# Performance work log

Measured on AMD Instinct MI355X. Metric: run time of the kernel, lower is better.

The kernel has to match this reference:

```python
import jax, jax.numpy as jnp
import numpy as np

EPS = 1e-12  # F.normalize eps


def _norm_adj(flow):
    # flow: (T, C, C). PyG gcn_norm with self-loops on the dense cosine-sim graph.
    T = flow.shape[0]
    x = flow.reshape(T, -1)                                  # (T, N)
    xn = x / jnp.clip(jnp.linalg.norm(x, axis=1, keepdims=True), EPS)
    A = xn.T @ xn                                            # (N, N) cosine sims
    N = A.shape[0]
    deg = A.sum(axis=0) + 1.0                                # +1 from added self-loop weight
    dinv = jnp.where(deg > 0, jax.lax.rsqrt(deg), 0.0)
    return (A + jnp.eye(N, dtype=A.dtype)) * dinv[:, None] * dinv[None, :]


def setup_inputs() -> dict:
    key = jax.random.key(0)
    ks = jax.random.split(key, 8)
    B, T, C, E = 8, 24, 64, 32
    H = 32
    O = 32
    return {
        "Flow": jax.random.normal(ks[0], (B, T, C, C), dtype=jnp.float32),
        "Edge": jax.random.normal(ks[1], (B, C, C, E), dtype=jnp.float32),
        "W0": jax.random.normal(ks[2], (E, H), dtype=jnp.float32) * 0.1,
        "b0": jax.random.normal(ks[3], (H,), dtype=jnp.float32) * 0.1,
        "W1": jax.random.normal(ks[4], (H, H), dtype=jnp.float32) * 0.1,
        "b1": jax.random.normal(ks[5], (H,), dtype=jnp.float32) * 0.1,
        "W2": jax.random.normal(ks[6], (H, O), dtype=jnp.float32) * 0.1,
        "b2": jax.random.normal(ks[7], (O,), dtype=jnp.float32) * 0.1,
    }


def reference(Flow, Edge, W0, b0, W1, b1, W2, b2):
    B, C, _, E = Edge.shape

    def per_batch(flow, edge):
        A = _norm_adj(flow)                                  # (N, N)
        x = edge.reshape(C * C, E)                           # (N, E)
        for W, b in ((W0, b0), (W1, b1), (W2, b2)):
            x = jax.nn.relu(A @ (x @ W) + b)
        return x.reshape(C, C, -1)

    return jax.vmap(per_batch)(Flow, Edge)                   # (B, C, C, out)
```

## Files before the change

kernel.cpp:

```cpp
#include <hip/hip_runtime.h>

#define BB 8
#define TT 24
#define NN 4096
#define HH 32
#define JT 64
#define UPB (TT*HH)

__global__ __launch_bounds__(256) void k_phase1(const float* __restrict__ Flow,
                                                const float* __restrict__ Edge,
                                                const float* __restrict__ W0,
                                                float* __restrict__ rn,
                                                float* __restrict__ s,
                                                float* __restrict__ u ,
                                                float* __restrict__ z0raw) {
    const int blk = blockIdx.x;
    const int tid = threadIdx.x;

    if (blk < BB * TT) {
        const float4* x = (const float4*)(Flow + (size_t)blk * NN);
        float sq = 0.f, sm = 0.f;
#pragma unroll
        for (int i = 0; i < 4; ++i) {
            float4 v = x[tid + i * 256];
            sq += v.x * v.x + v.y * v.y + v.z * v.z + v.w * v.w;
            sm += v.x + v.y + v.z + v.w;
        }
#pragma unroll
        for (int off = 32; off > 0; off >>= 1) {
            sq += __shfl_down(sq, off);
            sm += __shfl_down(sm, off);
        }
        __shared__ float rss[4], rsm[4];
        int wave = tid >> 6, lane = tid & 63;
        if (lane == 0) { rss[wave] = sq; rsm[wave] = sm; }
        __syncthreads();
        if (tid == 0) {
            float tss = rss[0] + rss[1] + rss[2] + rss[3];
            float tsm = rsm[0] + rsm[1] + rsm[2] + rsm[3];
            float r = 1.0f / fmaxf(sqrtf(tss), 1e-12f);
            rn[blk] = r;
            s[blk] = tsm * r;
        }
        int gid = blk * 256 + tid;
        if (gid < 3 * BB * TT * HH) u[gid] = 0.f;
    } else {
        const int g = blk - BB * TT;
        const int b = g >> 6;
        const int j0 = (g & 63) * JT;

        __shared__ float xs[JT][33];
        __shared__ float Ws[32][32];
        for (int i = tid; i < 1024; i += 256) Ws[i >> 5][i & 31] = W0[i];
        {
            const float4* eb = (const float4*)(Edge + ((size_t)b * NN + j0) * HH);
#pragma unroll
            for (int k = 0; k < 2; ++k) {
                int i = tid + k * 256;
                float4 v = eb[i];
                int r0 = i >> 3, c0 = (i & 7) * 4;
                xs[r0][c0] = v.x; xs[r0][c0 + 1] = v.y; xs[r0][c0 + 2] = v.z; xs[r0][c0 + 3] = v.w;
            }
        }
        __syncthreads();
        const int r = tid >> 2;
        const int h0 = (tid & 3) * 8;
        float zr[8];
#pragma unroll
        for (int hh = 0; hh < 8; ++hh) {
            float acc = 0.f;
#pragma unroll
            for (int e = 0; e < 32; ++e) acc += xs[r][e] * Ws[e][h0 + hh];
            zr[hh] = acc;
        }
        float* zb = z0raw + ((size_t)b * NN + j0 + r) * HH + h0;
        ((float4*)zb)[0] = make_float4(zr[0], zr[1], zr[2], zr[3]);
        ((float4*)zb)[1] = make_float4(zr[4], zr[5], zr[6], zr[7]);
    }
}

__global__ __launch_bounds__(256) void k_dinvU0(const float* __restrict__ Flow,
                                                const float* __restrict__ rn,
                                                const float* __restrict__ s,
                                                const float* __restrict__ z0raw,
                                                float* __restrict__ dinv,
                                                float* __restrict__ u0) {
    const int blk = blockIdx.x;
    const int b = blk >> 6;
    const int j0 = (blk & 63) * JT;
    const int tid = threadIdx.x;

    __shared__ float xns[TT][JT];
    __shared__ float zs[JT][33];
    __shared__ float sS[TT];

    if (tid < TT) sS[tid] = s[b * TT + tid];
    {
        const float4* zt = (const float4*)(z0raw + ((size_t)b * NN + j0) * HH);
#pragma unroll
        for (int k = 0; k < 2; ++k) {
            int i = tid + k * 256;
            float4 v = zt[i];
            int r0 = i >> 3, c0 = (i & 7) * 4;
            zs[r0][c0] = v.x; zs[r0][c0 + 1] = v.y; zs[r0][c0 + 2] = v.z; zs[r0][c0 + 3] = v.w;
        }
    }
    {
        const float* flb = Flow + (size_t)b * TT * NN + j0;
        for (int i = tid; i < TT * (JT / 4); i += 256) {
            int t = i >> 4, c0 = (i & 15) * 4;
            float4 v = ((const float4*)(flb + t * NN))[i & 15];
            float rt = rn[b * TT + t];
            xns[t][c0] = v.x * rt; xns[t][c0 + 1] = v.y * rt;
            xns[t][c0 + 2] = v.z * rt; xns[t][c0 + 3] = v.w * rt;
        }
    }
    __syncthreads();

    const int r = tid >> 2;
    const int h0 = (tid & 3) * 8;
    float deg = 1.0f;
#pragma unroll
    for (int t = 0; t < TT; ++t) deg += xns[t][r] * sS[t];
    const float di = (deg > 0.f) ? rsqrtf(deg) : 0.f;
    if ((tid & 3) == 0) dinv[b * NN + j0 + r] = di;
#pragma unroll
    for (int hh = 0; hh < 8; ++hh) zs[r][h0 + hh] *= di;
    __syncthreads();

#pragma unroll
    for (int k = 0; k < 3; ++k) {
        int p = tid + k * 256;
        int t = p >> 5, h = p & 31;
        float acc = 0.f;
#pragma unroll 8
        for (int rr = 0; rr < JT; ++rr) acc += xns[t][rr] * zs[rr][h];
        atomicAdd(&u0[(b * TT + t) * HH + h], acc);
    }
}

__global__ __launch_bounds__(256) void k_BA(const float* __restrict__ zraw_in,
                                            const float* __restrict__ Flow,
                                            const float* __restrict__ rn,
                                            const float* __restrict__ u_in,
                                            const float* __restrict__ dinv,
                                            const float* __restrict__ bias,
                                            const float* __restrict__ W,
                                            float* __restrict__ zraw_out,
                                            float* __restrict__ u_out) {
    const int blk = blockIdx.x;
    const int b = blk >> 6;
    const int j0 = (blk & 63) * JT;
    const int tid = threadIdx.x;

    __shared__ float us[TT][32];
    __shared__ float xns[TT][JT];
    __shared__ float Ws[32][32];
    __shared__ float xs[JT][33];
    __shared__ float zs[JT][33];
    __shared__ float bs[32];

    if (tid < 32) bs[tid] = bias[tid];
    for (int i = tid; i < 1024; i += 256) Ws[i >> 5][i & 31] = W[i];
    if (tid < UPB / 4) {
        float4 v = ((const float4*)(u_in + b * UPB))[tid];
        int t = tid >> 3, c0 = (tid & 7) * 4;
        us[t][c0] = v.x; us[t][c0 + 1] = v.y; us[t][c0 + 2] = v.z; us[t][c0 + 3] = v.w;
    }
    {
        const float4* zt = (const float4*)(zraw_in + ((size_t)b * NN + j0) * HH);
#pragma unroll
        for (int k = 0; k < 2; ++k) {
            int i = tid + k * 256;
            float4 v = zt[i];
            int r0 = i >> 3, c0 = (i & 7) * 4;
            zs[r0][c0] = v.x; zs[r0][c0 + 1] = v.y; zs[r0][c0 + 2] = v.z; zs[r0][c0 + 3] = v.w;
        }
    }
    {
        const float* flb = Flow + (size_t)b * TT * NN + j0;
        for (int i = tid; i < TT * (JT / 4); i += 256) {
            int t = i >> 4, c0 = (i & 15) * 4;
            float4 v = ((const float4*)(flb + t * NN))[i & 15];
            float rt = rn[b * TT + t];
            xns[t][c0] = v.x * rt; xns[t][c0 + 1] = v.y * rt;
            xns[t][c0 + 2] = v.z * rt; xns[t][c0 + 3] = v.w * rt;
        }
    }
    const int r = tid >> 2;
    const int h0 = (tid & 3) * 8;
    const float di = dinv[b * NN + j0 + r];
    __syncthreads();

    float zreg[8];
#pragma unroll
    for (int hh = 0; hh < 8; ++hh) zreg[hh] = di * zs[r][h0 + hh];
#pragma unroll
    for (int hh = 0; hh < 8; ++hh) {
        int h = h0 + hh;
        float acc = 0.f;
#pragma unroll
        for (int t = 0; t < TT; ++t) acc += xns[t][r] * us[t][h];
        xs[r][h] = fmaxf(di * (acc + zreg[hh]) + bs[h], 0.f);
    }
    float zr[8];
#pragma unroll
    for (int hh = 0; hh < 8; ++hh) {
        float acc = 0.f;
#pragma unroll
        for (int e = 0; e < 32; ++e) acc += xs[r][e] * Ws[e][h0 + hh];
        zr[hh] = acc;
        zs[r][h0 + hh] = di * zr[hh];
    }
    float* zb = zraw_out + ((size_t)b * NN + j0 + r) * HH + h0;
    ((float4*)zb)[0] = make_float4(zr[0], zr[1], zr[2], zr[3]);
    ((float4*)zb)[1] = make_float4(zr[4], zr[5], zr[6], zr[7]);
    __syncthreads();

#pragma unroll
    for (int k = 0; k < 3; ++k) {
        int p = tid + k * 256;
        int t = p >> 5, h = p & 31;
        float acc = 0.f;
#pragma unroll 8
        for (int rr = 0; rr < JT; ++rr) acc += xns[t][rr] * zs[rr][h];
        atomicAdd(&u_out[(b * TT + t) * HH + h], acc);
    }
}

__global__ __launch_bounds__(256) void k_Bfin(const float* __restrict__ zraw_in,
                                              const float* __restrict__ Flow,
                                              const float* __restrict__ rn,
                                              const float* __restrict__ u_in,
                                              const float* __restrict__ dinv,
                                              const float* __restrict__ bias,
                                              float* __restrict__ out) {
    const int blk = blockIdx.x;
    const int b = blk >> 6;
    const int j0 = (blk & 63) * JT;
    const int tid = threadIdx.x;

    __shared__ float us[TT][32];
    __shared__ float xns[TT][JT];
    __shared__ float bs[32];

    if (tid < 32) bs[tid] = bias[tid];
    if (tid < UPB / 4) {
        float4 v = ((const float4*)(u_in + b * UPB))[tid];
        int t = tid >> 3, c0 = (tid & 7) * 4;
        us[t][c0] = v.x; us[t][c0 + 1] = v.y; us[t][c0 + 2] = v.z; us[t][c0 + 3] = v.w;
    }
    {
        const float* flb = Flow + (size_t)b * TT * NN + j0;
        for (int i = tid; i < TT * (JT / 4); i += 256) {
            int t = i >> 4, c0 = (i & 15) * 4;
            float4 v = ((const float4*)(flb + t * NN))[i & 15];
            float rt = rn[b * TT + t];
            xns[t][c0] = v.x * rt; xns[t][c0 + 1] = v.y * rt;
            xns[t][c0 + 2] = v.z * rt; xns[t][c0 + 3] = v.w * rt;
        }
    }
    const int r = tid >> 2;
    const int h0 = (tid & 3) * 8;
    const float di = dinv[b * NN + j0 + r];
    const float* zrow = zraw_in + ((size_t)b * NN + j0 + r) * HH + h0;
    float4 zv0 = ((const float4*)zrow)[0];
    float4 zv1 = ((const float4*)zrow)[1];
    __syncthreads();

    float zreg[8] = { di * zv0.x, di * zv0.y, di * zv0.z, di * zv0.w,
                      di * zv1.x, di * zv1.y, di * zv1.z, di * zv1.w };
    float o[8];
#pragma unroll
    for (int hh = 0; hh < 8; ++hh) {
        int h = h0 + hh;
        float acc = 0.f;
#pragma unroll
        for (int t = 0; t < TT; ++t) acc += xns[t][r] * us[t][h];
        o[hh] = fmaxf(di * (acc + zreg[hh]) + bs[h], 0.f);
    }
    float* orow = out + ((size_t)b * NN + j0 + r) * HH + h0;
    ((float4*)orow)[0] = make_float4(o[0], o[1], o[2], o[3]);
    ((float4*)orow)[1] = make_float4(o[4], o[5], o[6], o[7]);
}

extern "C" void kernel_launch(void* const* d_in, const int* in_sizes, int n_in,
                              void* d_out, int out_size, void* d_ws, size_t ws_size,
                              hipStream_t stream) {
    const float* Flow = (const float*)d_in[0];
    const float* Edge = (const float*)d_in[1];
    const float* W0 = (const float*)d_in[2];
    const float* b0 = (const float*)d_in[3];
    const float* W1 = (const float*)d_in[4];
    const float* b1 = (const float*)d_in[5];
    const float* W2 = (const float*)d_in[6];
    const float* b2 = (const float*)d_in[7];
    float* out = (float*)d_out;

    float* ws = (float*)d_ws;
    float* rn   = ws;
    float* s    = rn + BB * TT;
    float* dinv = s + BB * TT;
    float* zA   = dinv + (size_t)BB * NN;
    float* zB   = zA + (size_t)BB * NN * HH;
    float* u    = zB + (size_t)BB * NN * HH;
    float* u0 = u, *u1 = u + BB * TT * HH, *u2 = u + 2 * BB * TT * HH;

    k_phase1<<<dim3(BB * TT + 512), 256, 0, stream>>>(Flow, Edge, W0, rn, s, u, zA);
    k_dinvU0<<<dim3(512), 256, 0, stream>>>(Flow, rn, s, zA, dinv, u0);
    k_BA<<<dim3(512), 256, 0, stream>>>(zA, Flow, rn, u0, dinv, b0, W1, zB, u1);
    k_BA<<<dim3(512), 256, 0, stream>>>(zB, Flow, rn, u1, dinv, b1, W2, zA, u2);
    k_Bfin<<<dim3(512), 256, 0, stream>>>(zA, Flow, rn, u2, dinv, b2, out);
}
```

Measured before the change: 43.07 us.

## Fuse layer kernels into one persistent kernel with per-batch grid barriers

Replaces the dinv/U0, two BA, and final kernels with a single kernel. It keeps Flow-normalised tiles, z rows and weights resident in shared memory and synchronises the 64 blocks of each batch through atomic counters between layers. This removes three kernel launches and the global round-trips for z and dinv. In exchange it needs all 512 blocks to be co-resident, otherwise the spin barrier can deadlock, and it adds barrier spin latency.

```diff
diff --git a/kernel.cpp b/kernel.cpp
--- a/kernel.cpp
+++ b/kernel.cpp
@@ -6,13 +6,14 @@
 #define HH 32
 #define JT 64
 #define UPB (TT*HH)
+#define CTRS 16
 
 __global__ __launch_bounds__(256) void k_phase1(const float* __restrict__ Flow,
                                                 const float* __restrict__ Edge,
                                                 const float* __restrict__ W0,
                                                 float* __restrict__ rn,
                                                 float* __restrict__ s,
-                                                float* __restrict__ u ,
+                                                float* __restrict__ uz ,
                                                 float* __restrict__ z0raw) {
     const int blk = blockIdx.x;
     const int tid = threadIdx.x;
@@ -43,7 +44,7 @@
             s[blk] = tsm * r;
         }
         int gid = blk * 256 + tid;
-        if (gid < 3 * BB * TT * HH) u[gid] = 0.f;
+        if (gid < 3 * BB * TT * HH + 3 * BB * CTRS) uz[gid] = 0.f;
     } else {
         const int g = blk - BB * TT;
         const int b = g >> 6;
@@ -79,12 +80,18 @@
     }
 }
 
-__global__ __launch_bounds__(256) void k_dinvU0(const float* __restrict__ Flow,
-                                                const float* __restrict__ rn,
-                                                const float* __restrict__ s,
-                                                const float* __restrict__ z0raw,
-                                                float* __restrict__ dinv,
-                                                float* __restrict__ u0) {
+__global__ __launch_bounds__(256) void k_mega(const float* __restrict__ Flow,
+                                              const float* __restrict__ z0raw,
+                                              const float* __restrict__ rn,
+                                              const float* __restrict__ s,
+                                              const float* __restrict__ W1,
+                                              const float* __restrict__ W2,
+                                              const float* __restrict__ b0,
+                                              const float* __restrict__ b1,
+                                              const float* __restrict__ b2,
+                                              float* __restrict__ u,
+                                              unsigned* __restrict__ ctr,
+                                              float* __restrict__ out) {
     const int blk = blockIdx.x;
     const int b = blk >> 6;
     const int j0 = (blk & 63) * JT;
@@ -92,9 +99,16 @@
 
     __shared__ float xns[TT][JT];
     __shared__ float zs[JT][33];
+    __shared__ float xs[JT][33];
+    __shared__ float W1s[32][32];
+    __shared__ float W2s[32][32];
+    __shared__ float us[TT][32];
     __shared__ float sS[TT];
+    __shared__ float b0s[32], b1s[32], b2s[32];
 
     if (tid < TT) sS[tid] = s[b * TT + tid];
+    if (tid < 32) { b0s[tid] = b0[tid]; b1s[tid] = b1[tid]; b2s[tid] = b2[tid]; }
+    for (int i = tid; i < 1024; i += 256) { W1s[i >> 5][i & 31] = W1[i]; W2s[i >> 5][i & 31] = W2[i]; }
     {
         const float4* zt = (const float4*)(z0raw + ((size_t)b * NN + j0) * HH);
 #pragma unroll
@@ -123,153 +137,94 @@
 #pragma unroll
     for (int t = 0; t < TT; ++t) deg += xns[t][r] * sS[t];
     const float di = (deg > 0.f) ? rsqrtf(deg) : 0.f;
-    if ((tid & 3) == 0) dinv[b * NN + j0 + r] = di;
 #pragma unroll
     for (int hh = 0; hh < 8; ++hh) zs[r][h0 + hh] *= di;
     __syncthreads();
 
-#pragma unroll
-    for (int k = 0; k < 3; ++k) {
-        int p = tid + k * 256;
-        int t = p >> 5, h = p & 31;
-        float acc = 0.f;
-#pragma unroll 8
-        for (int rr = 0; rr < JT; ++rr) acc += xns[t][rr] * zs[rr][h];
-        atomicAdd(&u0[(b * TT + t) * HH + h], acc);
-    }
-}
-
-__global__ __launch_bounds__(256) void k_BA(const float* __restrict__ zraw_in,
-                                            const float* __restrict__ Flow,
-                                            const float* __restrict__ rn,
-                                            const float* __restrict__ u_in,
-                                            const float* __restrict__ dinv,
-                                            const float* __restrict__ bias,
-                                            const float* __restrict__ W,
-                                            float* __restrict__ zraw_out,
-                                            float* __restrict__ u_out) {
-    const int blk = blockIdx.x;
-    const int b = blk >> 6;
-    const int j0 = (blk & 63) * JT;
-    const int tid = threadIdx.x;
-
-    __shared__ float us[TT][32];
-    __shared__ float xns[TT][JT];
-    __shared__ float Ws[32][32];
-    __shared__ float xs[JT][33];
-    __shared__ float zs[JT][33];
-    __shared__ float bs[32];
-
-    if (tid < 32) bs[tid] = bias[tid];
-    for (int i = tid; i < 1024; i += 256) Ws[i >> 5][i & 31] = W[i];
-    if (tid < UPB / 4) {
-        float4 v = ((const float4*)(u_in + b * UPB))[tid];
-        int t = tid >> 3, c0 = (tid & 7) * 4;
-        us[t][c0] = v.x; us[t][c0 + 1] = v.y; us[t][c0 + 2] = v.z; us[t][c0 + 3] = v.w;
-    }
-    {
-        const float4* zt = (const float4*)(zraw_in + ((size_t)b * NN + j0) * HH);
-#pragma unroll
-        for (int k = 0; k < 2; ++k) {
-            int i = tid + k * 256;
-            float4 v = zt[i];
-            int r0 = i >> 3, c0 = (i & 7) * 4;
-            zs[r0][c0] = v.x; zs[r0][c0 + 1] = v.y; zs[r0][c0 + 2] = v.z; zs[r0][c0 + 3] = v.w;
-        }
-    }
-    {
-        const float* flb = Flow + (size_t)b * TT * NN + j0;
-        for (int i = tid; i < TT * (JT / 4); i += 256) {
-            int t = i >> 4, c0 = (i & 15) * 4;
-            float4 v = ((const float4*)(flb + t * NN))[i & 15];
-            float rt = rn[b * TT + t];
-            xns[t][c0] = v.x * rt; xns[t][c0 + 1] = v.y * rt;
-            xns[t][c0 + 2] = v.z * rt; xns[t][c0 + 3] = v.w * rt;
-        }
-    }
-    const int r = tid >> 2;
-    const int h0 = (tid & 3) * 8;
-    const float di = dinv[b * NN + j0 + r];
-    __syncthreads();
-
-    float zreg[8];
-#pragma unroll
-    for (int hh = 0; hh < 8; ++hh) zreg[hh] = di * zs[r][h0 + hh];
+    float* u0 = u + b * UPB;
+    float* u1 = u0 + BB * UPB;
+    float* u2 = u1 + BB * UPB;
+
+#define U_PART(dst)                                                        \
+    {                                                                      \
+        _Pragma("unroll")                                                  \
+        for (int k = 0; k < 3; ++k) {                                      \
+            int p = tid + k * 256;                                         \
+            int t = p >> 5, h = p & 31;                                    \
+            float acc = 0.f;                                               \
+            _Pragma("unroll 8")                                            \
+            for (int rr = 0; rr < JT; ++rr) acc += xns[t][rr] * zs[rr][h]; \
+            atomicAdd(&(dst)[t * HH + h], acc);                            \
+        }                                                                  \
+    }
+
+#define BAR(phase)                                                                  \
+    {                                                                               \
+        __syncthreads();        \
+        if (tid == 0) {                                                             \
+            unsigned* c = ctr + ((phase) * BB + b) * CTRS;                          \
+            __hip_atomic_fetch_add(c, 1u, __ATOMIC_RELEASE, __HIP_MEMORY_SCOPE_AGENT); \
+            while (__hip_atomic_load(c, __ATOMIC_ACQUIRE, __HIP_MEMORY_SCOPE_AGENT) < 64u) \
+                __builtin_amdgcn_s_sleep(2);                                        \
+        }                                                                           \
+        __syncthreads();                                                            \
+    }
+
+#define LOAD_US(src)                                                                \
+    {                                                                               \
+        _Pragma("unroll")                                                           \
+        for (int k = 0; k < 3; ++k) {                                               \
+            int p = tid + k * 256;                                                  \
+            us[p >> 5][p & 31] = __hip_atomic_load(&(src)[p], __ATOMIC_RELAXED,     \
+                                                   __HIP_MEMORY_SCOPE_AGENT);       \
+        }                                                                           \
+        __syncthreads();                                                            \
+    }
+
+    U_PART(u0);
+    BAR(0);
+    LOAD_US(u0);
+
 #pragma unroll
     for (int hh = 0; hh < 8; ++hh) {
         int h = h0 + hh;
         float acc = 0.f;
 #pragma unroll
         for (int t = 0; t < TT; ++t) acc += xns[t][r] * us[t][h];
-        xs[r][h] = fmaxf(di * (acc + zreg[hh]) + bs[h], 0.f);
-    }
-    float zr[8];
-#pragma unroll
-    for (int hh = 0; hh < 8; ++hh) {
-        float acc = 0.f;
-#pragma unroll
-        for (int e = 0; e < 32; ++e) acc += xs[r][e] * Ws[e][h0 + hh];
-        zr[hh] = acc;
-        zs[r][h0 + hh] = di * zr[hh];
-    }
-    float* zb = zraw_out + ((size_t)b * NN + j0 + r) * HH + h0;
-    ((float4*)zb)[0] = make_float4(zr[0], zr[1], zr[2], zr[3]);
-    ((float4*)zb)[1] = make_float4(zr[4], zr[5], zr[6], zr[7]);
-    __syncthreads();
-
-#pragma unroll
-    for (int k = 0; k < 3; ++k) {
-        int p = tid + k * 256;
-        int t = p >> 5, h = p & 31;
-        float acc = 0.f;
-#pragma unroll 8
-        for (int rr = 0; rr < JT; ++rr) acc += xns[t][rr] * zs[rr][h];
-        atomicAdd(&u_out[(b * TT + t) * HH + h], acc);
-    }
-}
-
-__global__ __launch_bounds__(256) void k_Bfin(const float* __restrict__ zraw_in,
-                                              const float* __restrict__ Flow,
-                                              const float* __restrict__ rn,
-                                              const float* __restrict__ u_in,
-                                              const float* __restrict__ dinv,
-                                              const float* __restrict__ bias,
-                                              float* __restrict__ out) {
-    const int blk = blockIdx.x;
-    const int b = blk >> 6;
-    const int j0 = (blk & 63) * JT;
-    const int tid = threadIdx.x;
-
-    __shared__ float us[TT][32];
-    __shared__ float xns[TT][JT];
-    __shared__ float bs[32];
-
-    if (tid < 32) bs[tid] = bias[tid];
-    if (tid < UPB / 4) {
-        float4 v = ((const float4*)(u_in + b * UPB))[tid];
-        int t = tid >> 3, c0 = (tid & 7) * 4;
-        us[t][c0] = v.x; us[t][c0 + 1] = v.y; us[t][c0 + 2] = v.z; us[t][c0 + 3] = v.w;
-    }
-    {
-        const float* flb = Flow + (size_t)b * TT * NN + j0;
-        for (int i = tid; i < TT * (JT / 4); i += 256) {
-            int t = i >> 4, c0 = (i & 15) * 4;
-            float4 v = ((const float4*)(flb + t * NN))[i & 15];
-            float rt = rn[b * TT + t];
-            xns[t][c0] = v.x * rt; xns[t][c0 + 1] = v.y * rt;
-            xns[t][c0 + 2] = v.z * rt; xns[t][c0 + 3] = v.w * rt;
-        }
-    }
-    const int r = tid >> 2;
-    const int h0 = (tid & 3) * 8;
-    const float di = dinv[b * NN + j0 + r];
-    const float* zrow = zraw_in + ((size_t)b * NN + j0 + r) * HH + h0;
-    float4 zv0 = ((const float4*)zrow)[0];
-    float4 zv1 = ((const float4*)zrow)[1];
-    __syncthreads();
-
-    float zreg[8] = { di * zv0.x, di * zv0.y, di * zv0.z, di * zv0.w,
-                      di * zv1.x, di * zv1.y, di * zv1.z, di * zv1.w };
+        xs[r][h] = fmaxf(di * (acc + zs[r][h]) + b0s[h], 0.f);
+    }
+#pragma unroll
+    for (int hh = 0; hh < 8; ++hh) {
+        float acc = 0.f;
+#pragma unroll
+        for (int e = 0; e < 32; ++e) acc += xs[r][e] * W1s[e][h0 + hh];
+        zs[r][h0 + hh] = di * acc;
+    }
+    __syncthreads();
+    U_PART(u1);
+    BAR(1);
+    LOAD_US(u1);
+
+#pragma unroll
+    for (int hh = 0; hh < 8; ++hh) {
+        int h = h0 + hh;
+        float acc = 0.f;
+#pragma unroll
+        for (int t = 0; t < TT; ++t) acc += xns[t][r] * us[t][h];
+        xs[r][h] = fmaxf(di * (acc + zs[r][h]) + b1s[h], 0.f);
+    }
+#pragma unroll
+    for (int hh = 0; hh < 8; ++hh) {
+        float acc = 0.f;
+#pragma unroll
+        for (int e = 0; e < 32; ++e) acc += xs[r][e] * W2s[e][h0 + hh];
+        zs[r][h0 + hh] = di * acc;
+    }
+    __syncthreads();
+    U_PART(u2);
+    BAR(2);
+    LOAD_US(u2);
+
     float o[8];
 #pragma unroll
     for (int hh = 0; hh < 8; ++hh) {
@@ -277,11 +232,15 @@
         float acc = 0.f;
 #pragma unroll
         for (int t = 0; t < TT; ++t) acc += xns[t][r] * us[t][h];
-        o[hh] = fmaxf(di * (acc + zreg[hh]) + bs[h], 0.f);
+        o[hh] = fmaxf(di * (acc + zs[r][h]) + b2s[h], 0.f);
     }
     float* orow = out + ((size_t)b * NN + j0 + r) * HH + h0;
     ((float4*)orow)[0] = make_float4(o[0], o[1], o[2], o[3]);
     ((float4*)orow)[1] = make_float4(o[4], o[5], o[6], o[7]);
+
+#undef U_PART
+#undef BAR
+#undef LOAD_US
 }
 
 extern "C" void kernel_launch(void* const* d_in, const int* in_sizes, int n_in,
@@ -298,17 +257,13 @@
     float* out = (float*)d_out;
 
     float* ws = (float*)d_ws;
-    float* rn   = ws;
-    float* s    = rn + BB * TT;
-    float* dinv = s + BB * TT;
-    float* zA   = dinv + (size_t)BB * NN;
-    float* zB   = zA + (size_t)BB * NN * HH;
-    float* u    = zB + (size_t)BB * NN * HH;
-    float* u0 = u, *u1 = u + BB * TT * HH, *u2 = u + 2 * BB * TT * HH;
-
-    k_phase1<<<dim3(BB * TT + 512), 256, 0, stream>>>(Flow, Edge, W0, rn, s, u, zA);
-    k_dinvU0<<<dim3(512), 256, 0, stream>>>(Flow, rn, s, zA, dinv, u0);
-    k_BA<<<dim3(512), 256, 0, stream>>>(zA, Flow, rn, u0, dinv, b0, W1, zB, u1);
-    k_BA<<<dim3(512), 256, 0, stream>>>(zB, Flow, rn, u1, dinv, b1, W2, zA, u2);
-    k_Bfin<<<dim3(512), 256, 0, stream>>>(zA, Flow, rn, u2, dinv, b2, out);
+    float* rn    = ws;
+    float* s     = rn + BB * TT;
+    float* z0raw = s + BB * TT;
+    float* u     = z0raw + (size_t)BB * NN * HH;
+    unsigned* ctr = (unsigned*)(u + 3 * BB * UPB);
+
+    k_phase1<<<dim3(BB * TT + 512), 256, 0, stream>>>(Flow, Edge, W0, rn, s, u, z0raw);
+    k_mega<<<dim3(512), 256, 0, stream>>>(Flow, z0raw, rn, s, W1, W2, b0, b1, b2,
+                                          u, ctr, out);
 }
```

Result: slower. 74.01 us (+71.9%).

## Fuse last two layer kernels using per-batch grid barrier via atomic counters

Applied to the files above, without the earlier changes.

Merges the final k_BA launch and k_Bfin into one kernel. A per-batch atomic counter acts as a spin barrier so all 64 blocks of a batch finish accumulating u2 before any block reads it. This removes one kernel launch and the global round trip of the layer-2 z values, which now stay in shared memory. In exchange it depends on all 512 blocks being co-resident (hence launch_bounds(256,2)), and the spin has a bounded timeout that could silently yield wrong results if that does not hold.

```diff
diff --git a/kernel.cpp b/kernel.cpp
--- a/kernel.cpp
+++ b/kernel.cpp
@@ -6,13 +6,14 @@
 #define HH 32
 #define JT 64
 #define UPB (TT*HH)
+#define CTRS 16
 
 __global__ __launch_bounds__(256) void k_phase1(const float* __restrict__ Flow,
                                                 const float* __restrict__ Edge,
                                                 const float* __restrict__ W0,
                                                 float* __restrict__ rn,
                                                 float* __restrict__ s,
-                                                float* __restrict__ u ,
+                                                float* __restrict__ uz ,
                                                 float* __restrict__ z0raw) {
     const int blk = blockIdx.x;
     const int tid = threadIdx.x;
@@ -43,7 +44,7 @@
             s[blk] = tsm * r;
         }
         int gid = blk * 256 + tid;
-        if (gid < 3 * BB * TT * HH) u[gid] = 0.f;
+        if (gid < 3 * BB * TT * HH + BB * CTRS) uz[gid] = 0.f;
     } else {
         const int g = blk - BB * TT;
         const int b = g >> 6;
@@ -228,13 +229,17 @@
     }
 }
 
-__global__ __launch_bounds__(256) void k_Bfin(const float* __restrict__ zraw_in,
-                                              const float* __restrict__ Flow,
-                                              const float* __restrict__ rn,
-                                              const float* __restrict__ u_in,
-                                              const float* __restrict__ dinv,
-                                              const float* __restrict__ bias,
-                                              float* __restrict__ out) {
+__global__ __launch_bounds__(256, 2) void k_BAfin(const float* __restrict__ zraw_in,
+                                                  const float* __restrict__ Flow,
+                                                  const float* __restrict__ rn,
+                                                  const float* __restrict__ u_in,
+                                                  const float* __restrict__ dinv,
+                                                  const float* __restrict__ bias1,
+                                                  const float* __restrict__ W2,
+                                                  const float* __restrict__ bias2,
+                                                  float* __restrict__ u2,
+                                                  unsigned* __restrict__ ctr,
+                                                  float* __restrict__ out) {
     const int blk = blockIdx.x;
     const int b = blk >> 6;
     const int j0 = (blk & 63) * JT;
@@ -242,13 +247,27 @@
 
     __shared__ float us[TT][32];
     __shared__ float xns[TT][JT];
-    __shared__ float bs[32];
-
-    if (tid < 32) bs[tid] = bias[tid];
+    __shared__ float Ws[32][32];
+    __shared__ float xs[JT][33];
+    __shared__ float zs[JT][33];
+    __shared__ float b1s[32], b2s[32];
+
+    if (tid < 32) { b1s[tid] = bias1[tid]; b2s[tid] = bias2[tid]; }
+    for (int i = tid; i < 1024; i += 256) Ws[i >> 5][i & 31] = W2[i];
     if (tid < UPB / 4) {
         float4 v = ((const float4*)(u_in + b * UPB))[tid];
         int t = tid >> 3, c0 = (tid & 7) * 4;
         us[t][c0] = v.x; us[t][c0 + 1] = v.y; us[t][c0 + 2] = v.z; us[t][c0 + 3] = v.w;
+    }
+    {
+        const float4* zt = (const float4*)(zraw_in + ((size_t)b * NN + j0) * HH);
+#pragma unroll
+        for (int k = 0; k < 2; ++k) {
+            int i = tid + k * 256;
+            float4 v = zt[i];
+            int r0 = i >> 3, c0 = (i & 7) * 4;
+            zs[r0][c0] = v.x; zs[r0][c0 + 1] = v.y; zs[r0][c0 + 2] = v.z; zs[r0][c0 + 3] = v.w;
+        }
     }
     {
         const float* flb = Flow + (size_t)b * TT * NN + j0;
@@ -263,13 +282,56 @@
     const int r = tid >> 2;
     const int h0 = (tid & 3) * 8;
     const float di = dinv[b * NN + j0 + r];
-    const float* zrow = zraw_in + ((size_t)b * NN + j0 + r) * HH + h0;
-    float4 zv0 = ((const float4*)zrow)[0];
-    float4 zv1 = ((const float4*)zrow)[1];
-    __syncthreads();
-
-    float zreg[8] = { di * zv0.x, di * zv0.y, di * zv0.z, di * zv0.w,
-                      di * zv1.x, di * zv1.y, di * zv1.z, di * zv1.w };
+    __syncthreads();
+
+    float zreg[8];
+#pragma unroll
+    for (int hh = 0; hh < 8; ++hh) zreg[hh] = di * zs[r][h0 + hh];
+#pragma unroll
+    for (int hh = 0; hh < 8; ++hh) {
+        int h = h0 + hh;
+        float acc = 0.f;
+#pragma unroll
+        for (int t = 0; t < TT; ++t) acc += xns[t][r] * us[t][h];
+        xs[r][h] = fmaxf(di * (acc + zreg[hh]) + b1s[h], 0.f);
+    }
+#pragma unroll
+    for (int hh = 0; hh < 8; ++hh) {
+        float acc = 0.f;
+#pragma unroll
+        for (int e = 0; e < 32; ++e) acc += xs[r][e] * Ws[e][h0 + hh];
+        zs[r][h0 + hh] = di * acc;
+    }
+    __syncthreads();
+
+#pragma unroll
+    for (int k = 0; k < 3; ++k) {
+        int p = tid + k * 256;
+        int t = p >> 5, h = p & 31;
+        float acc = 0.f;
+#pragma unroll 8
+        for (int rr = 0; rr < JT; ++rr) acc += xns[t][rr] * zs[rr][h];
+        atomicAdd(&u2[b * UPB + t * HH + h], acc);
+    }
+
+    __syncthreads();
+    if (tid == 0) {
+        unsigned* c = ctr + b * CTRS;
+        __hip_atomic_fetch_add(c, 1u, __ATOMIC_RELAXED, __HIP_MEMORY_SCOPE_AGENT);
+        int lim = 1 << 22;
+        while (__hip_atomic_load(c, __ATOMIC_RELAXED, __HIP_MEMORY_SCOPE_AGENT) < 64u && --lim)
+            __builtin_amdgcn_s_sleep(1);
+    }
+    __syncthreads();
+
+#pragma unroll
+    for (int k = 0; k < 3; ++k) {
+        int p = tid + k * 256;
+        us[p >> 5][p & 31] = __hip_atomic_load(&u2[b * UPB + p], __ATOMIC_RELAXED,
+                                               __HIP_MEMORY_SCOPE_AGENT);
+    }
+    __syncthreads();
+
     float o[8];
 #pragma unroll
     for (int hh = 0; hh < 8; ++hh) {
@@ -277,7 +339,7 @@
         float acc = 0.f;
 #pragma unroll
         for (int t = 0; t < TT; ++t) acc += xns[t][r] * us[t][h];
-        o[hh] = fmaxf(di * (acc + zreg[hh]) + bs[h], 0.f);
+        o[hh] = fmaxf(di * (acc + zs[r][h]) + b2s[h], 0.f);
     }
     float* orow = out + ((size_t)b * NN + j0 + r) * HH + h0;
     ((float4*)orow)[0] = make_float4(o[0], o[1], o[2], o[3]);
@@ -298,17 +360,18 @@
     float* out = (float*)d_out;
 
     float* ws = (float*)d_ws;
-    float* rn   = ws;
-    float* s    = rn + BB * TT;
-    float* dinv = s + BB * TT;
-    float* zA   = dinv + (size_t)BB * NN;
-    float* zB   = zA + (size_t)BB * NN * HH;
-    float* u    = zB + (size_t)BB * NN * HH;
-    float* u0 = u, *u1 = u + BB * TT * HH, *u2 = u + 2 * BB * TT * HH;
+    float* rn    = ws;
+    float* s     = rn + BB * TT;
+    float* dinv  = s + BB * TT;
+    float* zA    = dinv + (size_t)BB * NN;
+    float* zB    = zA + (size_t)BB * NN * HH;
+    float* u     = zB + (size_t)BB * NN * HH;
+    unsigned* ctr = (unsigned*)(u + 3 * BB * UPB);
+    float* u0 = u, *u1 = u + BB * UPB, *u2 = u + 2 * BB * UPB;
 
     k_phase1<<<dim3(BB * TT + 512), 256, 0, stream>>>(Flow, Edge, W0, rn, s, u, zA);
     k_dinvU0<<<dim3(512), 256, 0, stream>>>(Flow, rn, s, zA, dinv, u0);
     k_BA<<<dim3(512), 256, 0, stream>>>(zA, Flow, rn, u0, dinv, b0, W1, zB, u1);
-    k_BA<<<dim3(512), 256, 0, stream>>>(zB, Flow, rn, u1, dinv, b1, W2, zA, u2);
-    k_Bfin<<<dim3(512), 256, 0, stream>>>(zA, Flow, rn, u2, dinv, b2, out);
-}
+    k_BAfin<<<dim3(512), 256, 0, stream>>>(zB, Flow, rn, u1, dinv, b1, W2, b2,
+                                           u2, ctr, out);
+}
```

New measurement: 43.65 us. About the same (+1.4%).
